# Performance work log

Measured on AMD Instinct MI355X. Metric: run time of the kernel, lower is better.

Reference implementation:

```python
import jax, jax.numpy as jnp
import numpy as np
from jax import lax

B, T, D, L, H, F = 2, 128, 256, 8, 4, 2048  # batch, time, dim, max_chunk_len, nhead, dim_feedforward
THRESH = 0.5


def setup_inputs() -> dict:
    key = jax.random.key(0)
    ks = jax.random.split(key, 12)
    s = 0.02
    nrm = lambda k, sh, sc=s: jax.random.normal(k, sh, jnp.float32) * sc
    return {
        "frames": jax.random.normal(ks[0], (B, T, D), jnp.float32),
        "cls_token": jax.random.normal(ks[1], (D,), jnp.float32),
        "Wq": nrm(ks[2], (D, D)), "bq": jnp.zeros((D,), jnp.float32),
        "Wk": nrm(ks[3], (D, D)), "bk": jnp.zeros((D,), jnp.float32),
        "Wv": nrm(ks[4], (D, D)), "bv": jnp.zeros((D,), jnp.float32),
        "Wo": nrm(ks[5], (D, D)), "bo": jnp.zeros((D,), jnp.float32),
        "ln1_g": jnp.ones((D,), jnp.float32), "ln1_b": jnp.zeros((D,), jnp.float32),
        "ln2_g": jnp.ones((D,), jnp.float32), "ln2_b": jnp.zeros((D,), jnp.float32),
        "W1": nrm(ks[6], (D, F)), "b1f": jnp.zeros((F,), jnp.float32),
        "W2": nrm(ks[7], (F, D)), "b2f": jnp.zeros((D,), jnp.float32),
        "We1": nrm(ks[8], (D, D)), "be1": jnp.zeros((D,), jnp.float32),
        "We2": jax.random.normal(ks[9], (D,), jnp.float32) * 0.1,
        "be2": jnp.zeros((), jnp.float32),
    }


def reference(frames, cls_token, Wq, bq, Wk, bk, Wv, bv, Wo, bo,
              ln1_g, ln1_b, ln2_g, ln2_b, W1, b1f, W2, b2f,
              We1, be1, We2, be2):
    """Dynamic chunker: for each start index i, grow window 1..L over frames[i:],
    run a pre-norm TransformerEncoderLayer on [CLS, window], stop at first
    p_eoc > THRESH (or window cap). Emits CLS encodings per chunk.
    Returns (chunks [B,T,D] zero-padded, counts [B])."""
    Bq, Tq, Dq = frames.shape
    dh = Dq // H
    scale = 1.0 / np.sqrt(dh).astype(np.float32)

    def ln(x, g, b):
        m = jnp.mean(x, -1, keepdims=True)
        v = jnp.var(x, -1, keepdims=True)
        return (x - m) * lax.rsqrt(v + 1e-5) * g + b

    def enc_cls(seq, kp):
        # seq: (1+L, D); kp: (1+L,) True = padded key. norm_first encoder layer.
        S = seq.shape[0]
        h = ln(seq, ln1_g, ln1_b)
        q = (h @ Wq + bq).reshape(S, H, dh)
        k = (h @ Wk + bk).reshape(S, H, dh)
        v = (h @ Wv + bv).reshape(S, H, dh)
        scores = jnp.einsum('qhd,khd->hqk', q, k) * scale
        scores = jnp.where(kp[None, None, :], -1e30, scores)
        a = jax.nn.softmax(scores, axis=-1)
        o = jnp.einsum('hqk,khd->qhd', a, v).reshape(S, Dq)
        x = seq + o @ Wo + bo
        h2 = ln(x, ln2_g, ln2_b)
        x = x + jax.nn.relu(h2 @ W1 + b1f) @ W2 + b2f
        return x[0]  # CLS position

    pos = jnp.arange(L)
    ls = jnp.arange(1, L + 1)

    def run(fpad):  # fpad: (T+L, D), one sample
        def step(i, _):
            win = lax.dynamic_slice(fpad, (i, 0), (L, Dq))           # frames[i:i+L] (zero-padded past T)
            seq = jnp.concatenate([cls_token[None, :], win], 0)     # (1+L, D)
            base_pad = (i + pos) >= Tq                               # positions past end of sequence
            kp = jnp.concatenate(
                [jnp.zeros((L, 1), bool),
                 (pos[None, :] >= ls[:, None]) | base_pad[None, :]], 1)  # (L, 1+L) one mask per candidate len
            enc = jax.vmap(enc_cls, in_axes=(None, 0))(seq, kp)      # (L, D) candidate CLS encodings
            p = jax.nn.sigmoid(jax.nn.relu(enc @ We1 + be1) @ We2 + be2)  # (L,) eoc probs
            lmax = jnp.clip(Tq - i, 1, L)
            stop = (p > THRESH) & (ls <= lmax)
            lstar = jnp.where(stop.any(), jnp.argmax(stop) + 1, lmax)
            active = i < Tq
            chunk = jnp.where(active, enc[lstar - 1], jnp.zeros((Dq,), seq.dtype))
            i_new = jnp.where(active, i + lstar.astype(i.dtype), i)
            return i_new, (chunk, active)

        _, (chunks, act) = lax.scan(step, jnp.int32(0), None, length=Tq)
        return chunks, act

    fpadded = jnp.pad(frames, ((0, 0), (0, L), (0, 0)))
    chunks, act = jax.vmap(run)(fpadded)
    counts = act.sum(-1).astype(jnp.int32)
    return chunks, counts
```

## Files before the change

### kernel.cpp

```cpp
#include <hip/hip_runtime.h>

#define DEV __device__ __forceinline__

constexpr int Bc = 2, Tc = 128, Dc = 256, Lc = 8, Hc = 4, DH = 64, Fc = 2048;
constexpr float EPS = 1e-5f, SCALE = 0.125f;
constexpr int NROWS = Bc * Tc * Lc;
constexpr int SLAB = NROWS * Dc;

constexpr int OFF_K     = 0;
constexpr int OFF_VWOH  = OFF_K + Bc * Tc * Dc;
constexpr int OFF_QCLS  = OFF_VWOH + Bc * Tc * Hc * Dc;
constexpr int OFF_KCLS  = OFF_QCLS + Dc;
constexpr int OFF_VWOHC = OFF_KCLS + Dc;
constexpr int OFF_ENC   = OFF_VWOHC + Hc * Dc;
constexpr int OFF_Z     = OFF_ENC + SLAB;
constexpr int OFF_H2    = OFF_Z + NROWS;
constexpr int OFF_U     = OFF_H2 + SLAB;

constexpr int RB = 32;
constexpr int GSPLIT = 8;
constexpr int FS = Fc / GSPLIT;

DEV int imin(int a, int b) { return a < b ? a : b; }

DEV float blockReduceSum(float v, float* red) {
#pragma unroll
  for (int off = 32; off; off >>= 1) v += __shfl_down(v, off, 64);
  const int lane = threadIdx.x & 63;
  const int w = threadIdx.x >> 6;
  __syncthreads();
  if (lane == 0) red[w] = v;
  __syncthreads();
  return red[0] + red[1] + red[2] + red[3];
}

__global__ __launch_bounds__(256) void k_prep(
    const float* __restrict__ frames, const float* __restrict__ cls,
    const float* __restrict__ Wq, const float* __restrict__ bq,
    const float* __restrict__ Wk, const float* __restrict__ bk,
    const float* __restrict__ Wv, const float* __restrict__ bv,
    const float* __restrict__ Wo,
    const float* __restrict__ g1, const float* __restrict__ b1,
    float* __restrict__ ws) {
  __shared__ float hsm[Dc];
  __shared__ float vsm[Dc];
  __shared__ float red[4];
  const int d = threadIdx.x;
  const int r = blockIdx.x;

  const float x = (r < Bc * Tc) ? frames[r * Dc + d] : cls[d];
  const float s = blockReduceSum(x, red);
  const float m = s * (1.0f / Dc);
  const float c = x - m;
  const float var = blockReduceSum(c * c, red) * (1.0f / Dc);
  hsm[d] = c * (1.0f / sqrtf(var + EPS)) * g1[d] + b1[d];
  __syncthreads();

  float ka = bk[d], va = bv[d];
  for (int c2 = 0; c2 < Dc; ++c2) {
    const float h = hsm[c2];
    ka = fmaf(h, Wk[c2 * Dc + d], ka);
    va = fmaf(h, Wv[c2 * Dc + d], va);
  }
  if (r < Bc * Tc) ws[OFF_K + r * Dc + d] = ka;
  else             ws[OFF_KCLS + d] = ka;
  vsm[d] = va;
  __syncthreads();

#pragma unroll
  for (int hh = 0; hh < Hc; ++hh) {
    float acc = 0.f;
    for (int c2 = 0; c2 < DH; ++c2)
      acc = fmaf(vsm[hh * DH + c2], Wo[(hh * DH + c2) * Dc + d], acc);
    if (r < Bc * Tc) ws[OFF_VWOH + r * (Hc * Dc) + hh * Dc + d] = acc;
    else             ws[OFF_VWOHC + hh * Dc + d] = acc;
  }
  if (r == Bc * Tc) {
    float qa = bq[d];
    for (int c2 = 0; c2 < Dc; ++c2) qa = fmaf(hsm[c2], Wq[c2 * Dc + d], qa);
    ws[OFF_QCLS + d] = qa;
  }
}

__global__ __launch_bounds__(256) void k_attn(
    const float* __restrict__ cls, const float* __restrict__ bo,
    const float* __restrict__ g2, const float* __restrict__ b2,
    float* __restrict__ ws) {
  const int wg = blockIdx.x;
  const int i = wg & (Tc - 1);
  const int tid = threadIdx.x;
  const int lane = tid & 63;
  const int lmax = imin(Tc - i, Lc);

  __shared__ float sv[Hc][Lc + 1];
  __shared__ float aP[Lc][Hc][Lc + 1];
  __shared__ __align__(16) float redA[Lc][4];
  __shared__ __align__(16) float redB[Lc][4];

  {
    const int hh = tid >> 6;
    const float qv = ws[OFF_QCLS + hh * DH + lane];
    for (int j = 0; j <= Lc; ++j) {
      float p = 0.f;
      if (j == 0) p = qv * ws[OFF_KCLS + hh * DH + lane];
      else if (j - 1 < lmax) p = qv * ws[OFF_K + (wg + j - 1) * Dc + hh * DH + lane];
#pragma unroll
      for (int off = 32; off; off >>= 1) p += __shfl_down(p, off, 64);
      if (lane == 0) sv[hh][j] = p * SCALE;
    }
  }
  __syncthreads();

  if (tid < Lc * Hc) {
    const int l = (tid >> 2) + 1, h4 = tid & 3;
    if (l <= lmax) {
      float mx = -1e30f;
      for (int j = 0; j <= l; ++j) mx = fmaxf(mx, sv[h4][j]);
      float den = 0.f;
      for (int j = 0; j <= l; ++j) den += expf(sv[h4][j] - mx);
      const float inv = 1.f / den;
      for (int j = 0; j <= l; ++j) aP[l - 1][h4][j] = expf(sv[h4][j] - mx) * inv;
    }
  }
  __syncthreads();

  const int d = tid;
  float x0v[Lc];
  {
    const float base = cls[d] + bo[d];
#pragma unroll
    for (int l = 0; l < Lc; ++l) x0v[l] = base;
    for (int j = 0; j <= lmax; ++j) {
      const float* vwp = (j == 0) ? (ws + OFF_VWOHC)
                                  : (ws + OFF_VWOH + (wg + j - 1) * (Hc * Dc));
      for (int h4 = 0; h4 < Hc; ++h4) {
        const float w = vwp[h4 * Dc + d];
        const int lstart = (j == 0) ? 1 : j;
        for (int l = lstart; l <= lmax; ++l) x0v[l - 1] = fmaf(aP[l - 1][h4][j], w, x0v[l - 1]);
      }
    }
#pragma unroll
    for (int l = 0; l < Lc; ++l) {
      float p = x0v[l];
#pragma unroll
      for (int off = 32; off; off >>= 1) p += __shfl_down(p, off, 64);
      if (lane == 0) redA[l][tid >> 6] = p;
    }
  }
  __syncthreads();

  float mean[Lc];
  {
#pragma unroll
    for (int l = 0; l < Lc; ++l) {
      const float4 s4 = *(const float4*)redA[l];
      mean[l] = (s4.x + s4.y + s4.z + s4.w) * (1.f / Dc);
    }
#pragma unroll
    for (int l = 0; l < Lc; ++l) {
      const float cv = x0v[l] - mean[l];
      float p = cv * cv;
#pragma unroll
      for (int off = 32; off; off >>= 1) p += __shfl_down(p, off, 64);
      if (lane == 0) redB[l][tid >> 6] = p;
    }
  }
  __syncthreads();

  {
    const float g2d = g2[d], b2d = b2[d];
    for (int l = 1; l <= lmax; ++l) {
      const float4 s4 = *(const float4*)redB[l - 1];
      const float var = (s4.x + s4.y + s4.z + s4.w) * (1.f / Dc);
      const float rstd = 1.f / sqrtf(var + EPS);
      ws[OFF_H2 + (wg * Lc + l - 1) * Dc + d] = (x0v[l - 1] - mean[l - 1]) * rstd * g2d + b2d;
      ws[OFF_ENC + (wg * Lc + l - 1) * Dc + d] = x0v[l - 1];
    }
    for (int l = lmax + 1; l <= Lc; ++l) {
      ws[OFF_H2 + (wg * Lc + l - 1) * Dc + d] = 0.f;
      ws[OFF_ENC + (wg * Lc + l - 1) * Dc + d] = 0.f;
    }
  }
}

__global__ __launch_bounds__(256) void k_ffn(
    const float* __restrict__ W1, const float* __restrict__ b1f,
    const float* __restrict__ W2, float* __restrict__ ws) {
  const int rb = blockIdx.x >> 3;
  const int g = blockIdx.x & 7;
  const int r0 = rb * RB;
  const int tid = threadIdx.x;
  const int cg = tid & 63;
  const int rg = tid >> 6;

  __shared__ __align__(16) float h2s[RB][Dc];
  __shared__ __align__(16) float Ts[RB][FS];

#pragma unroll
  for (int it = 0; it < 8; ++it) {
    const int row = it * 4 + rg;
    *(float4*)&h2s[row][cg * 4] =
        *(const float4*)&ws[OFF_H2 + (r0 + row) * Dc + cg * 4];
  }
  __syncthreads();

  const int f0 = g * FS + cg * 4;
  float t[8][4];
  {
    const float4 bb = *(const float4*)&b1f[f0];
#pragma unroll
    for (int r = 0; r < 8; ++r) { t[r][0] = bb.x; t[r][1] = bb.y; t[r][2] = bb.z; t[r][3] = bb.w; }
  }
  {
    const float* Wp = W1 + f0;
    float4 wn[4];
#pragma unroll
    for (int k = 0; k < 4; ++k) wn[k] = *(const float4*)&Wp[k * Fc];
    for (int c = 0; c < Dc; c += 4) {
      float4 wc[4];
#pragma unroll
      for (int k = 0; k < 4; ++k) wc[k] = wn[k];
      {
        const float* Wn = Wp + imin(c + 4, Dc - 4) * Fc;
#pragma unroll
        for (int k = 0; k < 4; ++k) wn[k] = *(const float4*)&Wn[k * Fc];
      }
#pragma unroll
      for (int r = 0; r < 8; ++r) {
        const float4 h = *(const float4*)&h2s[rg * 8 + r][c];
        const float hv[4] = {h.x, h.y, h.z, h.w};
#pragma unroll
        for (int k = 0; k < 4; ++k) {
          t[r][0] = fmaf(hv[k], wc[k].x, t[r][0]);
          t[r][1] = fmaf(hv[k], wc[k].y, t[r][1]);
          t[r][2] = fmaf(hv[k], wc[k].z, t[r][2]);
          t[r][3] = fmaf(hv[k], wc[k].w, t[r][3]);
        }
      }
    }
  }
#pragma unroll
  for (int r = 0; r < 8; ++r) {
    float4 v;
    v.x = fmaxf(t[r][0], 0.f); v.y = fmaxf(t[r][1], 0.f);
    v.z = fmaxf(t[r][2], 0.f); v.w = fmaxf(t[r][3], 0.f);
    *(float4*)&Ts[rg * 8 + r][cg * 4] = v;
  }
  __syncthreads();

  float u[8][4];
#pragma unroll
  for (int r = 0; r < 8; ++r) { u[r][0] = 0.f; u[r][1] = 0.f; u[r][2] = 0.f; u[r][3] = 0.f; }
  {
    const float* Wp = W2 + g * FS * Dc + cg * 4;
    float4 wn[4];
#pragma unroll
    for (int k = 0; k < 4; ++k) wn[k] = *(const float4*)&Wp[k * Dc];
    for (int kk = 0; kk < FS; kk += 4) {
      float4 wc[4];
#pragma unroll
      for (int k = 0; k < 4; ++k) wc[k] = wn[k];
      {
        const float* Wn = Wp + imin(kk + 4, FS - 4) * Dc;
#pragma unroll
        for (int k = 0; k < 4; ++k) wn[k] = *(const float4*)&Wn[k * Dc];
      }
#pragma unroll
      for (int r = 0; r < 8; ++r) {
        const float4 a = *(const float4*)&Ts[rg * 8 + r][kk];
        const float av[4] = {a.x, a.y, a.z, a.w};
#pragma unroll
        for (int k = 0; k < 4; ++k) {
          u[r][0] = fmaf(av[k], wc[k].x, u[r][0]);
          u[r][1] = fmaf(av[k], wc[k].y, u[r][1]);
          u[r][2] = fmaf(av[k], wc[k].z, u[r][2]);
          u[r][3] = fmaf(av[k], wc[k].w, u[r][3]);
        }
      }
    }
  }
#pragma unroll
  for (int r = 0; r < 8; ++r) {
    float4 v; v.x = u[r][0]; v.y = u[r][1]; v.z = u[r][2]; v.w = u[r][3];
    *(float4*)&ws[OFF_U + (g * NROWS + r0 + rg * 8 + r) * Dc + cg * 4] = v;
  }
}

__global__ __launch_bounds__(512) void k_z(
    const float* __restrict__ b2f,
    const float* __restrict__ We1, const float* __restrict__ be1,
    const float* __restrict__ We2, const float* __restrict__ be2,
    float* __restrict__ ws) {
  const int wg = blockIdx.x;
  const int tid = threadIdx.x;
  const int wv = tid >> 6, lane = tid & 63;

  __shared__ __align__(16) float encs[Lc][Dc];
  __shared__ float zred[8][4];

  {
    const int r = tid >> 6;
    const int dg = (tid & 63) * 4;
    const int row = wg * Lc + r;
    float4 s = *(const float4*)&ws[OFF_U + (0 * NROWS + row) * Dc + dg];
#pragma unroll
    for (int g = 1; g < GSPLIT; ++g) {
      const float4 p = *(const float4*)&ws[OFF_U + (g * NROWS + row) * Dc + dg];
      s.x += p.x; s.y += p.y; s.z += p.z; s.w += p.w;
    }
    const float4 x0 = *(const float4*)&ws[OFF_ENC + row * Dc + dg];
    const float4 bb = *(const float4*)&b2f[dg];
    float4 e;
    e.x = (x0.x + s.x) + bb.x; e.y = (x0.y + s.y) + bb.y;
    e.z = (x0.z + s.z) + bb.z; e.w = (x0.w + s.w) + bb.w;
    *(float4*)&ws[OFF_ENC + row * Dc + dg] = e;
    *(float4*)&encs[r][dg] = e;
  }
  __syncthreads();

  {
    const int f = tid & 255;
    const int rh = tid >> 8;
    float gr[4];
    const float be1f = be1[f];
#pragma unroll
    for (int rr = 0; rr < 4; ++rr) gr[rr] = be1f;
    for (int c = 0; c < Dc; c += 4) {
      const float w0 = We1[(c + 0) * Dc + f];
      const float w1 = We1[(c + 1) * Dc + f];
      const float w2 = We1[(c + 2) * Dc + f];
      const float w3 = We1[(c + 3) * Dc + f];
#pragma unroll
      for (int rr = 0; rr < 4; ++rr) {
        const float4 e = *(const float4*)&encs[rh * 4 + rr][c];
        gr[rr] = fmaf(e.x, w0, gr[rr]);
        gr[rr] = fmaf(e.y, w1, gr[rr]);
        gr[rr] = fmaf(e.z, w2, gr[rr]);
        gr[rr] = fmaf(e.w, w3, gr[rr]);
      }
    }
    const float w2v = We2[f];
#pragma unroll
    for (int rr = 0; rr < 4; ++rr) {
      float p = fmaxf(gr[rr], 0.f) * w2v;
#pragma unroll
      for (int off = 32; off; off >>= 1) p += __shfl_down(p, off, 64);
      if (lane == 0) zred[wv][rr] = p;
    }
  }
  __syncthreads();
  if (tid < 8) {
    const int r = tid;
    const int wb = (r < 4) ? 0 : 4;
    const int rl = r & 3;
    const float z = ((zred[wb + 0][rl] + zred[wb + 1][rl]) + zred[wb + 2][rl]) +
                    zred[wb + 3][rl];
    ws[OFF_Z + wg * 8 + r] = z + be2[0];
  }
}

__global__ __launch_bounds__(512) void k_fused(
    const float* __restrict__ cls, const float* __restrict__ bo,
    const float* __restrict__ g2, const float* __restrict__ b2,
    const float* __restrict__ W1, const float* __restrict__ b1f,
    const float* __restrict__ W2, const float* __restrict__ b2f,
    const float* __restrict__ We1, const float* __restrict__ be1,
    const float* __restrict__ We2, const float* __restrict__ be2,
    float* __restrict__ ws) {
  const int wg = blockIdx.x;
  const int i = wg & (Tc - 1);
  const int tid = threadIdx.x;
  const int wv = tid >> 6, lane = tid & 63;
  const int lmax = imin(Tc - i, Lc);

  __shared__ __align__(16) float ts[8][2048];
  __shared__ __align__(16) float h2s[8][256];
  __shared__ __align__(16) float x0s[8][256];
  __shared__ __align__(16) float encs[8][256];
  __shared__ float sv[Hc][Lc + 1];
  __shared__ float aP[Lc][Hc][Lc + 1];
  __shared__ __align__(16) float redA[Lc][4];
  __shared__ __align__(16) float redB[Lc][4];
  __shared__ float zred[8][4];

  if (tid < 256) {
    const int hh = tid >> 6;
    const float qv = ws[OFF_QCLS + hh * DH + lane];
    for (int j = 0; j <= Lc; ++j) {
      float p = 0.f;
      if (j == 0) p = qv * ws[OFF_KCLS + hh * DH + lane];
      else if (j - 1 < lmax) p = qv * ws[OFF_K + (wg + j - 1) * Dc + hh * DH + lane];
#pragma unroll
      for (int off = 32; off; off >>= 1) p += __shfl_down(p, off, 64);
      if (lane == 0) sv[hh][j] = p * SCALE;
    }
  }
  __syncthreads();

  if (tid < Lc * Hc) {
    const int l = (tid >> 2) + 1, h4 = tid & 3;
    if (l <= lmax) {
      float mx = -1e30f;
      for (int j = 0; j <= l; ++j) mx = fmaxf(mx, sv[h4][j]);
      float den = 0.f;
      for (int j = 0; j <= l; ++j) den += expf(sv[h4][j] - mx);
      const float inv = 1.f / den;
      for (int j = 0; j <= l; ++j) aP[l - 1][h4][j] = expf(sv[h4][j] - mx) * inv;
    }
  }
  __syncthreads();

  float x0v[Lc];
  if (tid < 256) {
    const int d = tid;
    const float base = cls[d] + bo[d];
#pragma unroll
    for (int l = 0; l < Lc; ++l) x0v[l] = base;
    for (int j = 0; j <= lmax; ++j) {
      const float* vwp = (j == 0) ? (ws + OFF_VWOHC)
                                  : (ws + OFF_VWOH + (wg + j - 1) * (Hc * Dc));
      for (int h4 = 0; h4 < Hc; ++h4) {
        const float w = vwp[h4 * Dc + d];
        const int lstart = (j == 0) ? 1 : j;
        for (int l = lstart; l <= lmax; ++l) x0v[l - 1] = fmaf(aP[l - 1][h4][j], w, x0v[l - 1]);
      }
    }
#pragma unroll
    for (int l = 0; l < Lc; ++l) {
      float p = x0v[l];
#pragma unroll
      for (int off = 32; off; off >>= 1) p += __shfl_down(p, off, 64);
      if (lane == 0) redA[l][tid >> 6] = p;
    }
  }
  __syncthreads();

  float mean[Lc];
  if (tid < 256) {
#pragma unroll
    for (int l = 0; l < Lc; ++l) {
      const float4 s4 = *(const float4*)redA[l];
      mean[l] = (s4.x + s4.y + s4.z + s4.w) * (1.f / Dc);
    }
#pragma unroll
    for (int l = 0; l < Lc; ++l) {
      const float cv = x0v[l] - mean[l];
      float p = cv * cv;
#pragma unroll
      for (int off = 32; off; off >>= 1) p += __shfl_down(p, off, 64);
      if (lane == 0) redB[l][tid >> 6] = p;
    }
  }
  __syncthreads();

  if (tid < 256) {
    const int d = tid;
    const float g2d = g2[d], b2d = b2[d];
    for (int l = 1; l <= lmax; ++l) {
      const float4 s4 = *(const float4*)redB[l - 1];
      const float var = (s4.x + s4.y + s4.z + s4.w) * (1.f / Dc);
      const float rstd = 1.f / sqrtf(var + EPS);
      h2s[l - 1][d] = (x0v[l - 1] - mean[l - 1]) * rstd * g2d + b2d;
      x0s[l - 1][d] = x0v[l - 1];
    }
    for (int l = lmax + 1; l <= Lc; ++l) {
      h2s[l - 1][d] = 0.f;
      x0s[l - 1][d] = 0.f;
    }
  }
  __syncthreads();

  const int fg = tid * 4;
  float t[8][4];
  {
    const float4 bb = *(const float4*)&b1f[fg];
#pragma unroll
    for (int r = 0; r < 8; ++r) { t[r][0] = bb.x; t[r][1] = bb.y; t[r][2] = bb.z; t[r][3] = bb.w; }
  }
  for (int c = 0; c < Dc; c += 4) {
    float4 w1v[4];
#pragma unroll
    for (int k = 0; k < 4; ++k) w1v[k] = *(const float4*)&W1[(c + k) * Fc + fg];
#pragma unroll
    for (int r = 0; r < 8; ++r) {
      const float4 h = *(const float4*)&h2s[r][c];
      const float hv[4] = {h.x, h.y, h.z, h.w};
#pragma unroll
      for (int k = 0; k < 4; ++k) {
        t[r][0] = fmaf(hv[k], w1v[k].x, t[r][0]);
        t[r][1] = fmaf(hv[k], w1v[k].y, t[r][1]);
        t[r][2] = fmaf(hv[k], w1v[k].z, t[r][2]);
        t[r][3] = fmaf(hv[k], w1v[k].w, t[r][3]);
      }
    }
  }
#pragma unroll
  for (int r = 0; r < 8; ++r) {
    float4 v;
    v.x = fmaxf(t[r][0], 0.f); v.y = fmaxf(t[r][1], 0.f);
    v.z = fmaxf(t[r][2], 0.f); v.w = fmaxf(t[r][3], 0.f);
    *(float4*)&ts[r][fg] = v;
  }
  __syncthreads();

  const int d4 = lane * 4;
  float u[8][4];
#pragma unroll
  for (int r = 0; r < 8; ++r) { u[r][0] = 0.f; u[r][1] = 0.f; u[r][2] = 0.f; u[r][3] = 0.f; }
  for (int kk = 0; kk < 256; kk += 4) {
    const int kg = wv * 256 + kk;
    float4 w2v[4];
#pragma unroll
    for (int k = 0; k < 4; ++k) w2v[k] = *(const float4*)&W2[(kg + k) * Dc + d4];
#pragma unroll
    for (int r = 0; r < 8; ++r) {
      const float4 h = *(const float4*)&ts[r][kg];
      const float hv[4] = {h.x, h.y, h.z, h.w};
#pragma unroll
      for (int k = 0; k < 4; ++k) {
        u[r][0] = fmaf(hv[k], w2v[k].x, u[r][0]);
        u[r][1] = fmaf(hv[k], w2v[k].y, u[r][1]);
        u[r][2] = fmaf(hv[k], w2v[k].z, u[r][2]);
        u[r][3] = fmaf(hv[k], w2v[k].w, u[r][3]);
      }
    }
  }
  __syncthreads();

  float* redb = &ts[0][0];
#pragma unroll
  for (int r = 0; r < 8; ++r) {
    float4 v; v.x = u[r][0]; v.y = u[r][1]; v.z = u[r][2]; v.w = u[r][3];
    *(float4*)&redb[(wv * 8 + r) * 256 + d4] = v;
  }
  __syncthreads();

  {
    const int r = tid >> 6;
    const int dg = (tid & 63) * 4;
    float4 s = *(const float4*)&redb[(0 * 8 + r) * 256 + dg];
#pragma unroll
    for (int w = 1; w < 8; ++w) {
      const float4 p = *(const float4*)&redb[(w * 8 + r) * 256 + dg];
      s.x += p.x; s.y += p.y; s.z += p.z; s.w += p.w;
    }
    const float4 x0 = *(const float4*)&x0s[r][dg];
    const float4 bb = *(const float4*)&b2f[dg];
    float4 e;
    e.x = (x0.x + s.x) + bb.x; e.y = (x0.y + s.y) + bb.y;
    e.z = (x0.z + s.z) + bb.z; e.w = (x0.w + s.w) + bb.w;
    *(float4*)&ws[OFF_ENC + (wg * 8 + r) * Dc + dg] = e;
    *(float4*)&encs[r][dg] = e;
  }
  __syncthreads();

  {
    const int f = tid & 255;
    const int rh = tid >> 8;
    float g[4];
    const float be1f = be1[f];
#pragma unroll
    for (int rr = 0; rr < 4; ++rr) g[rr] = be1f;
    for (int c = 0; c < Dc; ++c) {
      const float w = We1[c * Dc + f];
#pragma unroll
      for (int rr = 0; rr < 4; ++rr) g[rr] = fmaf(encs[rh * 4 + rr][c], w, g[rr]);
    }
    const float w2 = We2[f];
#pragma unroll
    for (int rr = 0; rr < 4; ++rr) {
      float p = fmaxf(g[rr], 0.f) * w2;
#pragma unroll
      for (int off = 32; off; off >>= 1) p += __shfl_down(p, off, 64);
      if (lane == 0) zred[wv][rr] = p;
    }
  }
  __syncthreads();
  if (tid < 8) {
    const int r = tid;
    const int wb = (r < 4) ? 0 : 4;
    const int rl = r & 3;
    const float z = ((zred[wb + 0][rl] + zred[wb + 1][rl]) + zred[wb + 2][rl]) +
                    zred[wb + 3][rl];
    ws[OFF_Z + wg * 8 + r] = z + be2[0];
  }
}

__global__ __launch_bounds__(256) void k_emit(float* __restrict__ ws, float* __restrict__ out) {
  const int b = blockIdx.x;
  const int tid = threadIdx.x;
  __shared__ int lst[Tc];
  __shared__ int path[Tc];
  __shared__ int cnt_s;
  if (tid < Tc) {
    const int i = tid;
    const int lmax = imin(Tc - i, Lc);
    const float* z = ws + OFF_Z + (b * Tc + i) * Lc;
    int ls = lmax;
    for (int l = 1; l <= lmax; ++l) {
      if (z[l - 1] > 0.f) { ls = l; break; }
    }
    lst[tid] = ls;
  }
  __syncthreads();
  if (tid < 64) {
    const int a0 = lst[tid], a1 = lst[64 + tid];
    int cur = 0, s = 0;
    while (cur < Tc) {
      const int l = (cur < 64) ? __shfl(a0, cur, 64) : __shfl(a1, cur - 64, 64);
      if (tid == 0) path[s] = cur * Lc + l - 1;
      ++s;
      cur += l;
    }
    if (tid == 0) cnt_s = s;
  }
  __syncthreads();
  const int c = cnt_s;
  for (int s0 = 0; s0 < Tc; s0 += 8) {
    float v[8];
#pragma unroll
    for (int k = 0; k < 8; ++k) {
      const int s = s0 + k;
      v[k] = (s < c) ? ws[OFF_ENC + (b * Tc * Lc + path[s]) * Dc + tid] : 0.f;
    }
#pragma unroll
    for (int k = 0; k < 8; ++k) out[(b * Tc + s0 + k) * Dc + tid] = v[k];
  }
  if (tid == 0) out[Bc * Tc * Dc + b] = (float)c;
}

extern "C" void kernel_launch(void* const* d_in, const int* in_sizes, int n_in,
                              void* d_out, int out_size, void* d_ws, size_t ws_size,
                              hipStream_t stream) {
  const float* frames = (const float*)d_in[0];
  const float* cls    = (const float*)d_in[1];
  const float* Wq     = (const float*)d_in[2];
  const float* bq     = (const float*)d_in[3];
  const float* Wk     = (const float*)d_in[4];
  const float* bk     = (const float*)d_in[5];
  const float* Wv     = (const float*)d_in[6];
  const float* bv     = (const float*)d_in[7];
  const float* Wo     = (const float*)d_in[8];
  const float* bo     = (const float*)d_in[9];
  const float* g1     = (const float*)d_in[10];
  const float* b1     = (const float*)d_in[11];
  const float* g2     = (const float*)d_in[12];
  const float* b2     = (const float*)d_in[13];
  const float* W1     = (const float*)d_in[14];
  const float* b1f    = (const float*)d_in[15];
  const float* W2     = (const float*)d_in[16];
  const float* b2f    = (const float*)d_in[17];
  const float* We1    = (const float*)d_in[18];
  const float* be1    = (const float*)d_in[19];
  const float* We2    = (const float*)d_in[20];
  const float* be2    = (const float*)d_in[21];
  float* ws = (float*)d_ws;
  float* out = (float*)d_out;

  k_prep<<<Bc * Tc + 1, 256, 0, stream>>>(frames, cls, Wq, bq, Wk, bk, Wv, bv, Wo, g1, b1, ws);

  const size_t need = (size_t)(OFF_U + GSPLIT * NROWS * Dc) * sizeof(float);
  if (ws_size >= need) {
    k_attn<<<Bc * Tc, 256, 0, stream>>>(cls, bo, g2, b2, ws);
    k_ffn<<<(NROWS / RB) * GSPLIT, 256, 0, stream>>>(W1, b1f, W2, ws);
    k_z<<<Bc * Tc, 512, 0, stream>>>(b2f, We1, be1, We2, be2, ws);
  } else {
    k_fused<<<Bc * Tc, 512, 0, stream>>>(cls, bo, g2, b2, W1, b1f, W2, b2f, We1, be1, We2, be2, ws);
  }
  k_emit<<<Bc, 256, 0, stream>>>(ws, out);
}
```

Measured before the change: 249.4 us.

## Fuse all stages into one persistent cooperative kernel with grid syncs

Replaces the five separate kernel launches (prep, attn, ffn, z, emit) with a single cooperative kernel of 1024 (or 512) blocks. Each block loops over the tasks of each stage, and grid.sync separates the stages; the shared memory for all stages is held in one union. The FFN row block is halved to 16 rows so more tasks are available for the persistent grid, and the z stage now runs on 256 threads. The aim is to remove launch gaps and tail effects between stages, at the cost of grid-wide barrier overhead, twice as many weight re-reads in the FFN, and possible occupancy limits. A multi-kernel path is kept as a fallback if the cooperative launch fails.

```diff
diff --git a/kernel.cpp b/kernel.cpp
--- a/kernel.cpp
+++ b/kernel.cpp
@@ -1,4 +1,7 @@
 #include <hip/hip_runtime.h>
+#include <hip/hip_cooperative_groups.h>
+
+namespace cg = cooperative_groups;
 
 #define DEV __device__ __forceinline__
 
@@ -17,11 +20,20 @@
 constexpr int OFF_H2    = OFF_Z + NROWS;
 constexpr int OFF_U     = OFF_H2 + SLAB;
 
-constexpr int RB = 32;
+constexpr int RB = 16;
 constexpr int GSPLIT = 8;
 constexpr int FS = Fc / GSPLIT;
+constexpr int NTASK_FFN = (NROWS / RB) * GSPLIT;
 
 DEV int imin(int a, int b) { return a < b ? a : b; }
+
+struct SMa { float hsm[Dc]; float vsm[Dc]; float red[4]; };
+struct SMb { float sv[Hc][Lc + 1]; float aP[Lc][Hc][Lc + 1];
+             float redA[Lc][4]; float redB[Lc][4]; };
+struct SMc { float h2s[RB][Dc]; float Ts[RB][FS]; };
+struct SMd { float encs[Lc][Dc]; float zred[2][4][4]; };
+struct SMe { int lst[Tc]; int path[Tc]; int cnt; };
+union SMu { SMa a; SMb b; SMc c; SMd d; SMe e; };
 
 DEV float blockReduceSum(float v, float* red) {
 #pragma unroll
@@ -32,6 +44,387 @@
   if (lane == 0) red[w] = v;
   __syncthreads();
   return red[0] + red[1] + red[2] + red[3];
+}
+
+
+DEV void prep_task(int r, const float* __restrict__ frames, const float* __restrict__ cls,
+                   const float* __restrict__ Wq, const float* __restrict__ bq,
+                   const float* __restrict__ Wk, const float* __restrict__ bk,
+                   const float* __restrict__ Wv, const float* __restrict__ bv,
+                   const float* __restrict__ Wo,
+                   const float* __restrict__ g1, const float* __restrict__ b1,
+                   float* __restrict__ ws, SMa& s) {
+  const int d = threadIdx.x;
+  const float x = (r < Bc * Tc) ? frames[r * Dc + d] : cls[d];
+  const float sum = blockReduceSum(x, s.red);
+  const float m = sum * (1.0f / Dc);
+  const float c = x - m;
+  const float var = blockReduceSum(c * c, s.red) * (1.0f / Dc);
+  s.hsm[d] = c * (1.0f / sqrtf(var + EPS)) * g1[d] + b1[d];
+  __syncthreads();
+
+  float ka = bk[d], va = bv[d];
+  for (int c2 = 0; c2 < Dc; ++c2) {
+    const float h = s.hsm[c2];
+    ka = fmaf(h, Wk[c2 * Dc + d], ka);
+    va = fmaf(h, Wv[c2 * Dc + d], va);
+  }
+  if (r < Bc * Tc) ws[OFF_K + r * Dc + d] = ka;
+  else             ws[OFF_KCLS + d] = ka;
+  s.vsm[d] = va;
+  __syncthreads();
+
+#pragma unroll
+  for (int hh = 0; hh < Hc; ++hh) {
+    float acc = 0.f;
+    for (int c2 = 0; c2 < DH; ++c2)
+      acc = fmaf(s.vsm[hh * DH + c2], Wo[(hh * DH + c2) * Dc + d], acc);
+    if (r < Bc * Tc) ws[OFF_VWOH + r * (Hc * Dc) + hh * Dc + d] = acc;
+    else             ws[OFF_VWOHC + hh * Dc + d] = acc;
+  }
+  if (r == Bc * Tc) {
+    float qa = bq[d];
+    for (int c2 = 0; c2 < Dc; ++c2) qa = fmaf(s.hsm[c2], Wq[c2 * Dc + d], qa);
+    ws[OFF_QCLS + d] = qa;
+  }
+}
+
+DEV void attn_task(int wg, const float* __restrict__ cls, const float* __restrict__ bo,
+                   const float* __restrict__ g2, const float* __restrict__ b2,
+                   float* __restrict__ ws, SMb& s) {
+  const int i = wg & (Tc - 1);
+  const int tid = threadIdx.x;
+  const int lane = tid & 63;
+  const int lmax = imin(Tc - i, Lc);
+
+  {
+    const int hh = tid >> 6;
+    const float qv = ws[OFF_QCLS + hh * DH + lane];
+    for (int j = 0; j <= Lc; ++j) {
+      float p = 0.f;
+      if (j == 0) p = qv * ws[OFF_KCLS + hh * DH + lane];
+      else if (j - 1 < lmax) p = qv * ws[OFF_K + (wg + j - 1) * Dc + hh * DH + lane];
+#pragma unroll
+      for (int off = 32; off; off >>= 1) p += __shfl_down(p, off, 64);
+      if (lane == 0) s.sv[hh][j] = p * SCALE;
+    }
+  }
+  __syncthreads();
+
+  if (tid < Lc * Hc) {
+    const int l = (tid >> 2) + 1, h4 = tid & 3;
+    if (l <= lmax) {
+      float mx = -1e30f;
+      for (int j = 0; j <= l; ++j) mx = fmaxf(mx, s.sv[h4][j]);
+      float den = 0.f;
+      for (int j = 0; j <= l; ++j) den += expf(s.sv[h4][j] - mx);
+      const float inv = 1.f / den;
+      for (int j = 0; j <= l; ++j) s.aP[l - 1][h4][j] = expf(s.sv[h4][j] - mx) * inv;
+    }
+  }
+  __syncthreads();
+
+  const int d = tid;
+  float x0v[Lc];
+  {
+    const float base = cls[d] + bo[d];
+#pragma unroll
+    for (int l = 0; l < Lc; ++l) x0v[l] = base;
+    for (int j = 0; j <= lmax; ++j) {
+      const float* vwp = (j == 0) ? (ws + OFF_VWOHC)
+                                  : (ws + OFF_VWOH + (wg + j - 1) * (Hc * Dc));
+      for (int h4 = 0; h4 < Hc; ++h4) {
+        const float w = vwp[h4 * Dc + d];
+        const int lstart = (j == 0) ? 1 : j;
+        for (int l = lstart; l <= lmax; ++l) x0v[l - 1] = fmaf(s.aP[l - 1][h4][j], w, x0v[l - 1]);
+      }
+    }
+#pragma unroll
+    for (int l = 0; l < Lc; ++l) {
+      float p = x0v[l];
+#pragma unroll
+      for (int off = 32; off; off >>= 1) p += __shfl_down(p, off, 64);
+      if (lane == 0) s.redA[l][tid >> 6] = p;
+    }
+  }
+  __syncthreads();
+
+  float mean[Lc];
+  {
+#pragma unroll
+    for (int l = 0; l < Lc; ++l) {
+      const float4 s4 = *(const float4*)s.redA[l];
+      mean[l] = (s4.x + s4.y + s4.z + s4.w) * (1.f / Dc);
+    }
+#pragma unroll
+    for (int l = 0; l < Lc; ++l) {
+      const float cv = x0v[l] - mean[l];
+      float p = cv * cv;
+#pragma unroll
+      for (int off = 32; off; off >>= 1) p += __shfl_down(p, off, 64);
+      if (lane == 0) s.redB[l][tid >> 6] = p;
+    }
+  }
+  __syncthreads();
+
+  {
+    const float g2d = g2[d], b2d = b2[d];
+    for (int l = 1; l <= lmax; ++l) {
+      const float4 s4 = *(const float4*)s.redB[l - 1];
+      const float var = (s4.x + s4.y + s4.z + s4.w) * (1.f / Dc);
+      const float rstd = 1.f / sqrtf(var + EPS);
+      ws[OFF_H2 + (wg * Lc + l - 1) * Dc + d] = (x0v[l - 1] - mean[l - 1]) * rstd * g2d + b2d;
+      ws[OFF_ENC + (wg * Lc + l - 1) * Dc + d] = x0v[l - 1];
+    }
+    for (int l = lmax + 1; l <= Lc; ++l) {
+      ws[OFF_H2 + (wg * Lc + l - 1) * Dc + d] = 0.f;
+      ws[OFF_ENC + (wg * Lc + l - 1) * Dc + d] = 0.f;
+    }
+  }
+}
+
+DEV void ffn_task(int task, const float* __restrict__ W1, const float* __restrict__ b1f,
+                  const float* __restrict__ W2, float* __restrict__ ws, SMc& s) {
+  const int rb = task >> 3;
+  const int g = task & 7;
+  const int r0 = rb * RB;
+  const int tid = threadIdx.x;
+  const int cg = tid & 63;
+  const int rg = tid >> 6;
+
+#pragma unroll
+  for (int it = 0; it < 4; ++it) {
+    const int row = it * 4 + rg;
+    *(float4*)&s.h2s[row][cg * 4] =
+        *(const float4*)&ws[OFF_H2 + (r0 + row) * Dc + cg * 4];
+  }
+  __syncthreads();
+
+  const int f0 = g * FS + cg * 4;
+  float t[4][4];
+  {
+    const float4 bb = *(const float4*)&b1f[f0];
+#pragma unroll
+    for (int r = 0; r < 4; ++r) { t[r][0] = bb.x; t[r][1] = bb.y; t[r][2] = bb.z; t[r][3] = bb.w; }
+  }
+  {
+    const float* Wp = W1 + f0;
+    float4 wn[4];
+#pragma unroll
+    for (int k = 0; k < 4; ++k) wn[k] = *(const float4*)&Wp[k * Fc];
+    for (int c = 0; c < Dc; c += 4) {
+      float4 wc[4];
+#pragma unroll
+      for (int k = 0; k < 4; ++k) wc[k] = wn[k];
+      {
+        const float* Wn = Wp + imin(c + 4, Dc - 4) * Fc;
+#pragma unroll
+        for (int k = 0; k < 4; ++k) wn[k] = *(const float4*)&Wn[k * Fc];
+      }
+#pragma unroll
+      for (int r = 0; r < 4; ++r) {
+        const float4 h = *(const float4*)&s.h2s[rg * 4 + r][c];
+        const float hv[4] = {h.x, h.y, h.z, h.w};
+#pragma unroll
+        for (int k = 0; k < 4; ++k) {
+          t[r][0] = fmaf(hv[k], wc[k].x, t[r][0]);
+          t[r][1] = fmaf(hv[k], wc[k].y, t[r][1]);
+          t[r][2] = fmaf(hv[k], wc[k].z, t[r][2]);
+          t[r][3] = fmaf(hv[k], wc[k].w, t[r][3]);
+        }
+      }
+    }
+  }
+#pragma unroll
+  for (int r = 0; r < 4; ++r) {
+    float4 v;
+    v.x = fmaxf(t[r][0], 0.f); v.y = fmaxf(t[r][1], 0.f);
+    v.z = fmaxf(t[r][2], 0.f); v.w = fmaxf(t[r][3], 0.f);
+    *(float4*)&s.Ts[rg * 4 + r][cg * 4] = v;
+  }
+  __syncthreads();
+
+  float u[4][4];
+#pragma unroll
+  for (int r = 0; r < 4; ++r) { u[r][0] = 0.f; u[r][1] = 0.f; u[r][2] = 0.f; u[r][3] = 0.f; }
+  {
+    const float* Wp = W2 + g * FS * Dc + cg * 4;
+    float4 wn[4];
+#pragma unroll
+    for (int k = 0; k < 4; ++k) wn[k] = *(const float4*)&Wp[k * Dc];
+    for (int kk = 0; kk < FS; kk += 4) {
+      float4 wc[4];
+#pragma unroll
+      for (int k = 0; k < 4; ++k) wc[k] = wn[k];
+      {
+        const float* Wn = Wp + imin(kk + 4, FS - 4) * Dc;
+#pragma unroll
+        for (int k = 0; k < 4; ++k) wn[k] = *(const float4*)&Wn[k * Dc];
+      }
+#pragma unroll
+      for (int r = 0; r < 4; ++r) {
+        const float4 a = *(const float4*)&s.Ts[rg * 4 + r][kk];
+        const float av[4] = {a.x, a.y, a.z, a.w};
+#pragma unroll
+        for (int k = 0; k < 4; ++k) {
+          u[r][0] = fmaf(av[k], wc[k].x, u[r][0]);
+          u[r][1] = fmaf(av[k], wc[k].y, u[r][1]);
+          u[r][2] = fmaf(av[k], wc[k].z, u[r][2]);
+          u[r][3] = fmaf(av[k], wc[k].w, u[r][3]);
+        }
+      }
+    }
+  }
+#pragma unroll
+  for (int r = 0; r < 4; ++r) {
+    float4 v; v.x = u[r][0]; v.y = u[r][1]; v.z = u[r][2]; v.w = u[r][3];
+    *(float4*)&ws[OFF_U + (g * NROWS + r0 + rg * 4 + r) * Dc + cg * 4] = v;
+  }
+}
+
+DEV void z_task(int wg, const float* __restrict__ b2f,
+                const float* __restrict__ We1, const float* __restrict__ be1,
+                const float* __restrict__ We2, const float* __restrict__ be2,
+                float* __restrict__ ws, SMd& s) {
+  const int tid = threadIdx.x;
+  const int wv = tid >> 6, lane = tid & 63;
+
+#pragma unroll
+  for (int half = 0; half < 2; ++half) {
+    const int r = half * 4 + wv;
+    const int dg = lane * 4;
+    const int row = wg * Lc + r;
+    float4 sum = *(const float4*)&ws[OFF_U + (0 * NROWS + row) * Dc + dg];
+#pragma unroll
+    for (int g = 1; g < GSPLIT; ++g) {
+      const float4 p = *(const float4*)&ws[OFF_U + (g * NROWS + row) * Dc + dg];
+      sum.x += p.x; sum.y += p.y; sum.z += p.z; sum.w += p.w;
+    }
+    const float4 x0 = *(const float4*)&ws[OFF_ENC + row * Dc + dg];
+    const float4 bb = *(const float4*)&b2f[dg];
+    float4 e;
+    e.x = (x0.x + sum.x) + bb.x; e.y = (x0.y + sum.y) + bb.y;
+    e.z = (x0.z + sum.z) + bb.z; e.w = (x0.w + sum.w) + bb.w;
+    *(float4*)&ws[OFF_ENC + row * Dc + dg] = e;
+    *(float4*)&s.encs[r][dg] = e;
+  }
+  __syncthreads();
+
+  const int f = tid;
+  const float be1f = be1[f];
+  const float w2v = We2[f];
+#pragma unroll
+  for (int rh = 0; rh < 2; ++rh) {
+    float gr[4];
+#pragma unroll
+    for (int rr = 0; rr < 4; ++rr) gr[rr] = be1f;
+    for (int c = 0; c < Dc; c += 4) {
+      const float w0 = We1[(c + 0) * Dc + f];
+      const float w1 = We1[(c + 1) * Dc + f];
+      const float w2 = We1[(c + 2) * Dc + f];
+      const float w3 = We1[(c + 3) * Dc + f];
+#pragma unroll
+      for (int rr = 0; rr < 4; ++rr) {
+        const float4 e = *(const float4*)&s.encs[rh * 4 + rr][c];
+        gr[rr] = fmaf(e.x, w0, gr[rr]);
+        gr[rr] = fmaf(e.y, w1, gr[rr]);
+        gr[rr] = fmaf(e.z, w2, gr[rr]);
+        gr[rr] = fmaf(e.w, w3, gr[rr]);
+      }
+    }
+#pragma unroll
+    for (int rr = 0; rr < 4; ++rr) {
+      float p = fmaxf(gr[rr], 0.f) * w2v;
+#pragma unroll
+      for (int off = 32; off; off >>= 1) p += __shfl_down(p, off, 64);
+      if (lane == 0) s.zred[rh][wv][rr] = p;
+    }
+  }
+  __syncthreads();
+  if (tid < 8) {
+    const int r = tid;
+    const int rh = r >> 2, rl = r & 3;
+    const float z = ((s.zred[rh][0][rl] + s.zred[rh][1][rl]) + s.zred[rh][2][rl]) +
+                    s.zred[rh][3][rl];
+    ws[OFF_Z + wg * 8 + r] = z + be2[0];
+  }
+}
+
+DEV void emit_task(int b, float* __restrict__ ws, float* __restrict__ out, SMe& s) {
+  const int tid = threadIdx.x;
+  if (tid < Tc) {
+    const int i = tid;
+    const int lmax = imin(Tc - i, Lc);
+    const float* z = ws + OFF_Z + (b * Tc + i) * Lc;
+    int ls = lmax;
+    for (int l = 1; l <= lmax; ++l) {
+      if (z[l - 1] > 0.f) { ls = l; break; }
+    }
+    s.lst[tid] = ls;
+  }
+  __syncthreads();
+  if (tid < 64) {
+    const int a0 = s.lst[tid], a1 = s.lst[64 + tid];
+    int cur = 0, n = 0;
+    while (cur < Tc) {
+      const int l = (cur < 64) ? __shfl(a0, cur, 64) : __shfl(a1, cur - 64, 64);
+      if (tid == 0) s.path[n] = cur * Lc + l - 1;
+      ++n;
+      cur += l;
+    }
+    if (tid == 0) s.cnt = n;
+  }
+  __syncthreads();
+  const int c = s.cnt;
+  for (int s0 = 0; s0 < Tc; s0 += 8) {
+    float v[8];
+#pragma unroll
+    for (int k = 0; k < 8; ++k) {
+      const int st = s0 + k;
+      v[k] = (st < c) ? ws[OFF_ENC + (b * Tc * Lc + s.path[st]) * Dc + tid] : 0.f;
+    }
+#pragma unroll
+    for (int k = 0; k < 8; ++k) out[(b * Tc + s0 + k) * Dc + tid] = v[k];
+  }
+  if (tid == 0) out[Bc * Tc * Dc + b] = (float)c;
+}
+
+__global__ __launch_bounds__(256, 4) void k_all(
+    const float* __restrict__ frames, const float* __restrict__ cls,
+    const float* __restrict__ Wq, const float* __restrict__ bq,
+    const float* __restrict__ Wk, const float* __restrict__ bk,
+    const float* __restrict__ Wv, const float* __restrict__ bv,
+    const float* __restrict__ Wo, const float* __restrict__ bo,
+    const float* __restrict__ g1, const float* __restrict__ b1,
+    const float* __restrict__ g2, const float* __restrict__ b2,
+    const float* __restrict__ W1, const float* __restrict__ b1f,
+    const float* __restrict__ W2, const float* __restrict__ b2f,
+    const float* __restrict__ We1, const float* __restrict__ be1,
+    const float* __restrict__ We2, const float* __restrict__ be2,
+    float* __restrict__ ws, float* __restrict__ out) {
+  __shared__ __align__(16) SMu sm;
+  cg::grid_group grid = cg::this_grid();
+  const int bid = blockIdx.x;
+  const int NB = gridDim.x;
+
+  for (int r = bid; r <= Bc * Tc; r += NB)
+    prep_task(r, frames, cls, Wq, bq, Wk, bk, Wv, bv, Wo, g1, b1, ws, sm.a);
+  grid.sync();
+
+  for (int wg = bid; wg < Bc * Tc; wg += NB)
+    attn_task(wg, cls, bo, g2, b2, ws, sm.b);
+  grid.sync();
+
+  for (int task = bid; task < NTASK_FFN; task += NB)
+    ffn_task(task, W1, b1f, W2, ws, sm.c);
+  grid.sync();
+
+  for (int wg = bid; wg < Bc * Tc; wg += NB)
+    z_task(wg, b2f, We1, be1, We2, be2, ws, sm.d);
+  grid.sync();
+
+  for (int b = bid; b < Bc; b += NB)
+    emit_task(b, ws, out, sm.e);
 }
 
 __global__ __launch_bounds__(256) void k_prep(
@@ -42,321 +435,37 @@
     const float* __restrict__ Wo,
     const float* __restrict__ g1, const float* __restrict__ b1,
     float* __restrict__ ws) {
-  __shared__ float hsm[Dc];
-  __shared__ float vsm[Dc];
-  __shared__ float red[4];
-  const int d = threadIdx.x;
-  const int r = blockIdx.x;
-
-  const float x = (r < Bc * Tc) ? frames[r * Dc + d] : cls[d];
-  const float s = blockReduceSum(x, red);
-  const float m = s * (1.0f / Dc);
-  const float c = x - m;
-  const float var = blockReduceSum(c * c, red) * (1.0f / Dc);
-  hsm[d] = c * (1.0f / sqrtf(var + EPS)) * g1[d] + b1[d];
-  __syncthreads();
-
-  float ka = bk[d], va = bv[d];
-  for (int c2 = 0; c2 < Dc; ++c2) {
-    const float h = hsm[c2];
-    ka = fmaf(h, Wk[c2 * Dc + d], ka);
-    va = fmaf(h, Wv[c2 * Dc + d], va);
-  }
-  if (r < Bc * Tc) ws[OFF_K + r * Dc + d] = ka;
-  else             ws[OFF_KCLS + d] = ka;
-  vsm[d] = va;
-  __syncthreads();
-
-#pragma unroll
-  for (int hh = 0; hh < Hc; ++hh) {
-    float acc = 0.f;
-    for (int c2 = 0; c2 < DH; ++c2)
-      acc = fmaf(vsm[hh * DH + c2], Wo[(hh * DH + c2) * Dc + d], acc);
-    if (r < Bc * Tc) ws[OFF_VWOH + r * (Hc * Dc) + hh * Dc + d] = acc;
-    else             ws[OFF_VWOHC + hh * Dc + d] = acc;
-  }
-  if (r == Bc * Tc) {
-    float qa = bq[d];
-    for (int c2 = 0; c2 < Dc; ++c2) qa = fmaf(hsm[c2], Wq[c2 * Dc + d], qa);
-    ws[OFF_QCLS + d] = qa;
-  }
+  __shared__ __align__(16) SMa s;
+  prep_task(blockIdx.x, frames, cls, Wq, bq, Wk, bk, Wv, bv, Wo, g1, b1, ws, s);
 }
 
 __global__ __launch_bounds__(256) void k_attn(
     const float* __restrict__ cls, const float* __restrict__ bo,
     const float* __restrict__ g2, const float* __restrict__ b2,
     float* __restrict__ ws) {
-  const int wg = blockIdx.x;
-  const int i = wg & (Tc - 1);
-  const int tid = threadIdx.x;
-  const int lane = tid & 63;
-  const int lmax = imin(Tc - i, Lc);
-
-  __shared__ float sv[Hc][Lc + 1];
-  __shared__ float aP[Lc][Hc][Lc + 1];
-  __shared__ __align__(16) float redA[Lc][4];
-  __shared__ __align__(16) float redB[Lc][4];
-
-  {
-    const int hh = tid >> 6;
-    const float qv = ws[OFF_QCLS + hh * DH + lane];
-    for (int j = 0; j <= Lc; ++j) {
-      float p = 0.f;
-      if (j == 0) p = qv * ws[OFF_KCLS + hh * DH + lane];
-      else if (j - 1 < lmax) p = qv * ws[OFF_K + (wg + j - 1) * Dc + hh * DH + lane];
-#pragma unroll
-      for (int off = 32; off; off >>= 1) p += __shfl_down(p, off, 64);
-      if (lane == 0) sv[hh][j] = p * SCALE;
-    }
-  }
-  __syncthreads();
-
-  if (tid < Lc * Hc) {
-    const int l = (tid >> 2) + 1, h4 = tid & 3;
-    if (l <= lmax) {
-      float mx = -1e30f;
-      for (int j = 0; j <= l; ++j) mx = fmaxf(mx, sv[h4][j]);
-      float den = 0.f;
-      for (int j = 0; j <= l; ++j) den += expf(sv[h4][j] - mx);
-      const float inv = 1.f / den;
-      for (int j = 0; j <= l; ++j) aP[l - 1][h4][j] = expf(sv[h4][j] - mx) * inv;
-    }
-  }
-  __syncthreads();
-
-  const int d = tid;
-  float x0v[Lc];
-  {
-    const float base = cls[d] + bo[d];
-#pragma unroll
-    for (int l = 0; l < Lc; ++l) x0v[l] = base;
-    for (int j = 0; j <= lmax; ++j) {
-      const float* vwp = (j == 0) ? (ws + OFF_VWOHC)
-                                  : (ws + OFF_VWOH + (wg + j - 1) * (Hc * Dc));
-      for (int h4 = 0; h4 < Hc; ++h4) {
-        const float w = vwp[h4 * Dc + d];
-        const int lstart = (j == 0) ? 1 : j;
-        for (int l = lstart; l <= lmax; ++l) x0v[l - 1] = fmaf(aP[l - 1][h4][j], w, x0v[l - 1]);
-      }
-    }
-#pragma unroll
-    for (int l = 0; l < Lc; ++l) {
-      float p = x0v[l];
-#pragma unroll
-      for (int off = 32; off; off >>= 1) p += __shfl_down(p, off, 64);
-      if (lane == 0) redA[l][tid >> 6] = p;
-    }
-  }
-  __syncthreads();
-
-  float mean[Lc];
-  {
-#pragma unroll
-    for (int l = 0; l < Lc; ++l) {
-      const float4 s4 = *(const float4*)redA[l];
-      mean[l] = (s4.x + s4.y + s4.z + s4.w) * (1.f / Dc);
-    }
-#pragma unroll
-    for (int l = 0; l < Lc; ++l) {
-      const float cv = x0v[l] - mean[l];
-      float p = cv * cv;
-#pragma unroll
-      for (int off = 32; off; off >>= 1) p += __shfl_down(p, off, 64);
-      if (lane == 0) redB[l][tid >> 6] = p;
-    }
-  }
-  __syncthreads();
-
-  {
-    const float g2d = g2[d], b2d = b2[d];
-    for (int l = 1; l <= lmax; ++l) {
-      const float4 s4 = *(const float4*)redB[l - 1];
-      const float var = (s4.x + s4.y + s4.z + s4.w) * (1.f / Dc);
-      const float rstd = 1.f / sqrtf(var + EPS);
-      ws[OFF_H2 + (wg * Lc + l - 1) * Dc + d] = (x0v[l - 1] - mean[l - 1]) * rstd * g2d + b2d;
-      ws[OFF_ENC + (wg * Lc + l - 1) * Dc + d] = x0v[l - 1];
-    }
-    for (int l = lmax + 1; l <= Lc; ++l) {
-      ws[OFF_H2 + (wg * Lc + l - 1) * Dc + d] = 0.f;
-      ws[OFF_ENC + (wg * Lc + l - 1) * Dc + d] = 0.f;
-    }
-  }
-}
-
-__global__ __launch_bounds__(256) void k_ffn(
+  __shared__ __align__(16) SMb s;
+  attn_task(blockIdx.x, cls, bo, g2, b2, ws, s);
+}
+
+__global__ __launch_bounds__(256, 4) void k_ffn16(
     const float* __restrict__ W1, const float* __restrict__ b1f,
     const float* __restrict__ W2, float* __restrict__ ws) {
-  const int rb = blockIdx.x >> 3;
-  const int g = blockIdx.x & 7;
-  const int r0 = rb * RB;
-  const int tid = threadIdx.x;
-  const int cg = tid & 63;
-  const int rg = tid >> 6;
-
-  __shared__ __align__(16) float h2s[RB][Dc];
-  __shared__ __align__(16) float Ts[RB][FS];
-
-#pragma unroll
-  for (int it = 0; it < 8; ++it) {
-    const int row = it * 4 + rg;
-    *(float4*)&h2s[row][cg * 4] =
-        *(const float4*)&ws[OFF_H2 + (r0 + row) * Dc + cg * 4];
-  }
-  __syncthreads();
-
-  const int f0 = g * FS + cg * 4;
-  float t[8][4];
-  {
-    const float4 bb = *(const float4*)&b1f[f0];
-#pragma unroll
-    for (int r = 0; r < 8; ++r) { t[r][0] = bb.x; t[r][1] = bb.y; t[r][2] = bb.z; t[r][3] = bb.w; }
-  }
-  {
-    const float* Wp = W1 + f0;
-    float4 wn[4];
-#pragma unroll
-    for (int k = 0; k < 4; ++k) wn[k] = *(const float4*)&Wp[k * Fc];
-    for (int c = 0; c < Dc; c += 4) {
-      float4 wc[4];
-#pragma unroll
-      for (int k = 0; k < 4; ++k) wc[k] = wn[k];
-      {
-        const float* Wn = Wp + imin(c + 4, Dc - 4) * Fc;
-#pragma unroll
-        for (int k = 0; k < 4; ++k) wn[k] = *(const float4*)&Wn[k * Fc];
-      }
-#pragma unroll
-      for (int r = 0; r < 8; ++r) {
-        const float4 h = *(const float4*)&h2s[rg * 8 + r][c];
-        const float hv[4] = {h.x, h.y, h.z, h.w};
-#pragma unroll
-        for (int k = 0; k < 4; ++k) {
-          t[r][0] = fmaf(hv[k], wc[k].x, t[r][0]);
-          t[r][1] = fmaf(hv[k], wc[k].y, t[r][1]);
-          t[r][2] = fmaf(hv[k], wc[k].z, t[r][2]);
-          t[r][3] = fmaf(hv[k], wc[k].w, t[r][3]);
-        }
-      }
-    }
-  }
-#pragma unroll
-  for (int r = 0; r < 8; ++r) {
-    float4 v;
-    v.x = fmaxf(t[r][0], 0.f); v.y = fmaxf(t[r][1], 0.f);
-    v.z = fmaxf(t[r][2], 0.f); v.w = fmaxf(t[r][3], 0.f);
-    *(float4*)&Ts[rg * 8 + r][cg * 4] = v;
-  }
-  __syncthreads();
-
-  float u[8][4];
-#pragma unroll
-  for (int r = 0; r < 8; ++r) { u[r][0] = 0.f; u[r][1] = 0.f; u[r][2] = 0.f; u[r][3] = 0.f; }
-  {
-    const float* Wp = W2 + g * FS * Dc + cg * 4;
-    float4 wn[4];
-#pragma unroll
-    for (int k = 0; k < 4; ++k) wn[k] = *(const float4*)&Wp[k * Dc];
-    for (int kk = 0; kk < FS; kk += 4) {
-      float4 wc[4];
-#pragma unroll
-      for (int k = 0; k < 4; ++k) wc[k] = wn[k];
-      {
-        const float* Wn = Wp + imin(kk + 4, FS - 4) * Dc;
-#pragma unroll
-        for (int k = 0; k < 4; ++k) wn[k] = *(const float4*)&Wn[k * Dc];
-      }
-#pragma unroll
-      for (int r = 0; r < 8; ++r) {
-        const float4 a = *(const float4*)&Ts[rg * 8 + r][kk];
-        const float av[4] = {a.x, a.y, a.z, a.w};
-#pragma unroll
-        for (int k = 0; k < 4; ++k) {
-          u[r][0] = fmaf(av[k], wc[k].x, u[r][0]);
-          u[r][1] = fmaf(av[k], wc[k].y, u[r][1]);
-          u[r][2] = fmaf(av[k], wc[k].z, u[r][2]);
-          u[r][3] = fmaf(av[k], wc[k].w, u[r][3]);
-        }
-      }
-    }
-  }
-#pragma unroll
-  for (int r = 0; r < 8; ++r) {
-    float4 v; v.x = u[r][0]; v.y = u[r][1]; v.z = u[r][2]; v.w = u[r][3];
-    *(float4*)&ws[OFF_U + (g * NROWS + r0 + rg * 8 + r) * Dc + cg * 4] = v;
-  }
-}
-
-__global__ __launch_bounds__(512) void k_z(
+  __shared__ __align__(16) SMc s;
+  ffn_task(blockIdx.x, W1, b1f, W2, ws, s);
+}
+
+__global__ __launch_bounds__(256) void k_z(
     const float* __restrict__ b2f,
     const float* __restrict__ We1, const float* __restrict__ be1,
     const float* __restrict__ We2, const float* __restrict__ be2,
     float* __restrict__ ws) {
-  const int wg = blockIdx.x;
-  const int tid = threadIdx.x;
-  const int wv = tid >> 6, lane = tid & 63;
-
-  __shared__ __align__(16) float encs[Lc][Dc];
-  __shared__ float zred[8][4];
-
-  {
-    const int r = tid >> 6;
-    const int dg = (tid & 63) * 4;
-    const int row = wg * Lc + r;
-    float4 s = *(const float4*)&ws[OFF_U + (0 * NROWS + row) * Dc + dg];
-#pragma unroll
-    for (int g = 1; g < GSPLIT; ++g) {
-      const float4 p = *(const float4*)&ws[OFF_U + (g * NROWS + row) * Dc + dg];
-      s.x += p.x; s.y += p.y; s.z += p.z; s.w += p.w;
-    }
-    const float4 x0 = *(const float4*)&ws[OFF_ENC + row * Dc + dg];
-    const float4 bb = *(const float4*)&b2f[dg];
-    float4 e;
-    e.x = (x0.x + s.x) + bb.x; e.y = (x0.y + s.y) + bb.y;
-    e.z = (x0.z + s.z) + bb.z; e.w = (x0.w + s.w) + bb.w;
-    *(float4*)&ws[OFF_ENC + row * Dc + dg] = e;
-    *(float4*)&encs[r][dg] = e;
-  }
-  __syncthreads();
-
-  {
-    const int f = tid & 255;
-    const int rh = tid >> 8;
-    float gr[4];
-    const float be1f = be1[f];
-#pragma unroll
-    for (int rr = 0; rr < 4; ++rr) gr[rr] = be1f;
-    for (int c = 0; c < Dc; c += 4) {
-      const float w0 = We1[(c + 0) * Dc + f];
-      const float w1 = We1[(c + 1) * Dc + f];
-      const float w2 = We1[(c + 2) * Dc + f];
-      const float w3 = We1[(c + 3) * Dc + f];
-#pragma unroll
-      for (int rr = 0; rr < 4; ++rr) {
-        const float4 e = *(const float4*)&encs[rh * 4 + rr][c];
-        gr[rr] = fmaf(e.x, w0, gr[rr]);
-        gr[rr] = fmaf(e.y, w1, gr[rr]);
-        gr[rr] = fmaf(e.z, w2, gr[rr]);
-        gr[rr] = fmaf(e.w, w3, gr[rr]);
-      }
-    }
-    const float w2v = We2[f];
-#pragma unroll
-    for (int rr = 0; rr < 4; ++rr) {
-      float p = fmaxf(gr[rr], 0.f) * w2v;
-#pragma unroll
-      for (int off = 32; off; off >>= 1) p += __shfl_down(p, off, 64);
-      if (lane == 0) zred[wv][rr] = p;
-    }
-  }
-  __syncthreads();
-  if (tid < 8) {
-    const int r = tid;
-    const int wb = (r < 4) ? 0 : 4;
-    const int rl = r & 3;
-    const float z = ((zred[wb + 0][rl] + zred[wb + 1][rl]) + zred[wb + 2][rl]) +
-                    zred[wb + 3][rl];
-    ws[OFF_Z + wg * 8 + r] = z + be2[0];
-  }
+  __shared__ __align__(16) SMd s;
+  z_task(blockIdx.x, b2f, We1, be1, We2, be2, ws, s);
+}
+
+__global__ __launch_bounds__(256) void k_emit(float* __restrict__ ws, float* __restrict__ out) {
+  __shared__ __align__(16) SMe s;
+  emit_task(blockIdx.x, ws, out, s);
 }
 
 __global__ __launch_bounds__(512) void k_fused(
@@ -584,49 +693,6 @@
                     zred[wb + 3][rl];
     ws[OFF_Z + wg * 8 + r] = z + be2[0];
   }
-}
-
-__global__ __launch_bounds__(256) void k_emit(float* __restrict__ ws, float* __restrict__ out) {
-  const int b = blockIdx.x;
-  const int tid = threadIdx.x;
-  __shared__ int lst[Tc];
-  __shared__ int path[Tc];
-  __shared__ int cnt_s;
-  if (tid < Tc) {
-    const int i = tid;
-    const int lmax = imin(Tc - i, Lc);
-    const float* z = ws + OFF_Z + (b * Tc + i) * Lc;
-    int ls = lmax;
-    for (int l = 1; l <= lmax; ++l) {
-      if (z[l - 1] > 0.f) { ls = l; break; }
-    }
-    lst[tid] = ls;
-  }
-  __syncthreads();
-  if (tid < 64) {
-    const int a0 = lst[tid], a1 = lst[64 + tid];
-    int cur = 0, s = 0;
-    while (cur < Tc) {
-      const int l = (cur < 64) ? __shfl(a0, cur, 64) : __shfl(a1, cur - 64, 64);
-      if (tid == 0) path[s] = cur * Lc + l - 1;
-      ++s;
-      cur += l;
-    }
-    if (tid == 0) cnt_s = s;
-  }
-  __syncthreads();
-  const int c = cnt_s;
-  for (int s0 = 0; s0 < Tc; s0 += 8) {
-    float v[8];
-#pragma unroll
-    for (int k = 0; k < 8; ++k) {
-      const int s = s0 + k;
-      v[k] = (s < c) ? ws[OFF_ENC + (b * Tc * Lc + path[s]) * Dc + tid] : 0.f;
-    }
-#pragma unroll
-    for (int k = 0; k < 8; ++k) out[(b * Tc + s0 + k) * Dc + tid] = v[k];
-  }
-  if (tid == 0) out[Bc * Tc * Dc + b] = (float)c;
 }
 
 extern "C" void kernel_launch(void* const* d_in, const int* in_sizes, int n_in,
@@ -657,15 +723,31 @@
   float* ws = (float*)d_ws;
   float* out = (float*)d_out;
 
-  k_prep<<<Bc * Tc + 1, 256, 0, stream>>>(frames, cls, Wq, bq, Wk, bk, Wv, bv, Wo, g1, b1, ws);
-
   const size_t need = (size_t)(OFF_U + GSPLIT * NROWS * Dc) * sizeof(float);
+
   if (ws_size >= need) {
+    void* args[24] = {
+        (void*)&frames, (void*)&cls, (void*)&Wq, (void*)&bq, (void*)&Wk, (void*)&bk,
+        (void*)&Wv, (void*)&bv, (void*)&Wo, (void*)&bo, (void*)&g1, (void*)&b1,
+        (void*)&g2, (void*)&b2, (void*)&W1, (void*)&b1f, (void*)&W2, (void*)&b2f,
+        (void*)&We1, (void*)&be1, (void*)&We2, (void*)&be2, (void*)&ws, (void*)&out};
+    hipError_t e = hipLaunchCooperativeKernel((const void*)k_all, dim3(1024), dim3(256),
+                                              args, 0, stream);
+    if (e != hipSuccess) {
+      (void)hipGetLastError();
+      e = hipLaunchCooperativeKernel((const void*)k_all, dim3(512), dim3(256),
+                                     args, 0, stream);
+    }
+    if (e == hipSuccess) return;
+    (void)hipGetLastError();
+    k_prep<<<Bc * Tc + 1, 256, 0, stream>>>(frames, cls, Wq, bq, Wk, bk, Wv, bv, Wo, g1, b1, ws);
     k_attn<<<Bc * Tc, 256, 0, stream>>>(cls, bo, g2, b2, ws);
-    k_ffn<<<(NROWS / RB) * GSPLIT, 256, 0, stream>>>(W1, b1f, W2, ws);
-    k_z<<<Bc * Tc, 512, 0, stream>>>(b2f, We1, be1, We2, be2, ws);
+    k_ffn16<<<NTASK_FFN, 256, 0, stream>>>(W1, b1f, W2, ws);
+    k_z<<<Bc * Tc, 256, 0, stream>>>(b2f, We1, be1, We2, be2, ws);
+    k_emit<<<Bc, 256, 0, stream>>>(ws, out);
   } else {
+    k_prep<<<Bc * Tc + 1, 256, 0, stream>>>(frames, cls, Wq, bq, Wk, bk, Wv, bv, Wo, g1, b1, ws);
     k_fused<<<Bc * Tc, 512, 0, stream>>>(cls, bo, g2, b2, W1, b1f, W2, b2f, We1, be1, We2, be2, ws);
-  }
-  k_emit<<<Bc, 256, 0, stream>>>(ws, out);
-}
+    k_emit<<<Bc, 256, 0, stream>>>(ws, out);
+  }
+}
```

Result: slower. 913.1 us (+266.0%).
